# Kernel tuning notes

Hardware: AMD Instinct MI355X
Metric: run time of the kernel (lower is better)

The kernel has to match this reference:

```python
import jax, jax.numpy as jnp
import numpy as np

D_MODEL = 512
N_HEADS = 8
B, S = 2, 2048


def setup_inputs() -> dict:
    key = jax.random.key(0)
    ks = jax.random.split(key, 7)
    scale = 1.0 / np.sqrt(D_MODEL)
    return {
        "q": jax.random.normal(ks[0], (B, S, D_MODEL), jnp.float32),
        "k": jax.random.normal(ks[1], (B, S, D_MODEL), jnp.float32),
        "v": jax.random.normal(ks[2], (B, S, D_MODEL), jnp.float32),
        "Wq_w": jax.random.normal(ks[3], (D_MODEL, D_MODEL), jnp.float32) * scale,
        "Wq_b": jnp.zeros((D_MODEL,), jnp.float32),
        "Wc_w": jax.random.normal(ks[4], (D_MODEL, D_MODEL), jnp.float32) * scale,
        "Wc_b": jnp.zeros((D_MODEL,), jnp.float32),
    }


def _split(x, n_heads):
    b, s, d = x.shape
    return x.reshape(b, s, n_heads, d // n_heads).transpose(0, 2, 1, 3)  # [b,h,s,dh]


def reference(q, k, v, Wq_w, Wq_b, Wc_w, Wc_b):
    # NOTE: original code (faithfully) projects q, k, v all with W_q.
    qp = q @ Wq_w.T + Wq_b
    kp = k @ Wq_w.T + Wq_b
    vp = v @ Wq_w.T + Wq_b
    qh = _split(qp, N_HEADS)  # [b,h,s,dh]
    kh = _split(kp, N_HEADS)
    vh = _split(vp, N_HEADS)
    d_tensor = qh.shape[-1]
    scores = jnp.einsum("bhqd,bhkd->bhqk", qh, kh) / jnp.sqrt(jnp.float32(d_tensor))
    att = jax.nn.softmax(scores, axis=-1)
    out = jnp.einsum("bhqk,bhkd->bhqd", att, vh)
    b, h, s, dh = out.shape
    out = out.transpose(0, 2, 1, 3).reshape(b, s, h * dh)
    return out @ Wc_w.T + Wc_b
```

## Files before the change

kernel.cpp:

```cpp
#include <hip/hip_runtime.h>
#include <hip/hip_bf16.h>
#include <stdint.h>


typedef __bf16 bf16;
typedef __bf16 bvec8 __attribute__((ext_vector_type(8)));
typedef __bf16 bvec4 __attribute__((ext_vector_type(4)));
typedef float  fvec4 __attribute__((ext_vector_type(4)));
typedef float  fvec16 __attribute__((ext_vector_type(16)));
typedef int    ivec4 __attribute__((ext_vector_type(4)));

#define MFMA16(a, b, c) __builtin_amdgcn_mfma_f32_16x16x32_bf16(a, b, c, 0, 0, 0)
#define MFMA32(a, b, c) __builtin_amdgcn_mfma_f32_32x32x16_bf16(a, b, c, 0, 0, 0)

__device__ __forceinline__ void async16(const void* g, void* l) {
  __builtin_amdgcn_global_load_lds(
      (__attribute__((address_space(1))) void*)(g),
      (__attribute__((address_space(3))) void*)(l), 16, 0, 0);
}

__global__ void cvt_all(const float* __restrict__ q, const float* __restrict__ k,
                        const float* __restrict__ v, const float* __restrict__ Wq,
                        const float* __restrict__ Wc, bf16* __restrict__ qkvb,
                        bf16* __restrict__ Wq16, bf16* __restrict__ Wc16) {
  const int t = blockIdx.x * 256 + threadIdx.x;
  const float* src;
  bf16* dst;
  size_t i;
  if (t < 786432) {
    const int which = t >> 18;
    i = (size_t)(t & 262143);
    src = (which == 0) ? q : (which == 1) ? k : v;
    dst = qkvb + ((size_t)which << 21);
  } else if (t < 819200) {
    src = Wq; dst = Wq16; i = (size_t)(t - 786432);
  } else {
    src = Wc; dst = Wc16; i = (size_t)(t - 819200);
  }
  fvec4 a = *(const fvec4*)(src + i * 8);
  fvec4 b = *(const fvec4*)(src + i * 8 + 4);
  bvec8 o;
#pragma unroll
  for (int j = 0; j < 4; ++j) { o[j] = (bf16)a[j]; o[j + 4] = (bf16)b[j]; }
  *(bvec8*)(dst + i * 8) = o;
}

__launch_bounds__(256, 3)
__global__ void proj_gemm(const bf16* __restrict__ X, const bf16* __restrict__ W,
                          const float* __restrict__ bias, bf16* __restrict__ Y,
                          bf16* __restrict__ Yt) {
  __shared__ __attribute__((aligned(16))) char As[2][64 * 128];
  __shared__ __attribute__((aligned(16))) char Bs[2][128 * 128];

  const int tid = threadIdx.x;
  const int w = tid >> 6, l = tid & 63;
  const int wr = w >> 1, wc = w & 1;
  const int l15 = l & 15, lg = l >> 4;
  const int bm0 = blockIdx.x * 64;
  const int bn0 = blockIdx.y * 128;

  fvec4 acc[2][4] = {};

  auto stageA = [&](int buf, int k0) {
#pragma unroll
    for (int j = 0; j < 2; ++j) {
      int c = j * 256 + tid;
      int row = c >> 3, g = (c & 7) ^ (row & 7);
      async16(X + (size_t)(bm0 + row) * 512 + k0 + g * 8, &As[buf][c * 16]);
    }
  };
  auto stageB = [&](int buf, int k0) {
#pragma unroll
    for (int j = 0; j < 4; ++j) {
      int c = j * 256 + tid;
      int row = c >> 3, g = (c & 7) ^ (row & 7);
      async16(W + (size_t)(bn0 + row) * 512 + k0 + g * 8, &Bs[buf][c * 16]);
    }
  };

  stageA(0, 0);
  stageB(0, 0);
  __syncthreads();

  for (int t = 0; t < 8; ++t) {
    const int buf = t & 1;
    if (t < 7) { stageA(buf ^ 1, (t + 1) * 64); stageB(buf ^ 1, (t + 1) * 64); }
#pragma unroll
    for (int kk = 0; kk < 2; ++kk) {
      bvec8 af[2], bfr[4];
      const int g = kk * 4 + lg;
#pragma unroll
      for (int m = 0; m < 2; ++m) {
        int r = wr * 32 + m * 16 + l15;
        af[m] = *(const bvec8*)&As[buf][r * 128 + ((g ^ (r & 7)) << 4)];
      }
#pragma unroll
      for (int n = 0; n < 4; ++n) {
        int r = wc * 64 + n * 16 + l15;
        bfr[n] = *(const bvec8*)&Bs[buf][r * 128 + ((g ^ (r & 7)) << 4)];
      }
#pragma unroll
      for (int m = 0; m < 2; ++m)
#pragma unroll
        for (int n = 0; n < 4; ++n) acc[m][n] = MFMA16(af[m], bfr[n], acc[m][n]);
    }
    __syncthreads();
  }

  const bool trans = (bm0 >= 8192);
#pragma unroll
  for (int n = 0; n < 4; ++n) {
    const int col = bn0 + wc * 64 + n * 16 + l15;
    const float bv = bias[col];
#pragma unroll
    for (int m = 0; m < 2; ++m) {
      const int row0 = bm0 + wr * 32 + m * 16 + lg * 4;
      if (!trans) {
#pragma unroll
        for (int r = 0; r < 4; ++r)
          Y[(size_t)(row0 + r) * 512 + col] = (bf16)(acc[m][n][r] + bv);
      } else {
        const int m0 = row0 - 8192;
        const int b = m0 >> 11, s = m0 & 2047;
        bvec4 v4;
#pragma unroll
        for (int r = 0; r < 4; ++r) v4[r] = (bf16)(acc[m][n][r] + bv);
        *(bvec4*)&Yt[(size_t)(b * 512 + col) * 2048 + s] = v4;
      }
    }
  }
}

__launch_bounds__(256, 4)
__global__ void attn_kernel(const bf16* __restrict__ qp, const bf16* __restrict__ kp,
                            const bf16* __restrict__ vt, bf16* __restrict__ po01,
                            bf16* __restrict__ po23, float* __restrict__ pl) {
  __shared__ __attribute__((aligned(16))) char Ks[2][64 * 128];
  __shared__ __attribute__((aligned(16))) char Vs[2][64 * 128];

  const int tid = threadIdx.x;
  const int w = tid >> 6, l = tid & 63;
  const int l31 = l & 31, hi = l >> 5;

  const int lin = blockIdx.x;
  const int work = (lin & 7) * 128 + (lin >> 3);
  const int qb = work & 15, bh = (work >> 4) & 15, half = work >> 8;
  const int b = bh >> 3, h = bh & 7;
  const int kvbase = half * 512;
  const int qw0 = qb * 128 + w * 32;

  const bf16* kbase = kp + (size_t)(b * 2048) * 512 + h * 64;
  const bf16* vbase = vt + (size_t)(b * 512 + h * 64) * 2048;

  bvec8 qf[4];
  {
    const bf16* qrow = qp + (size_t)(b * 2048 + qw0 + l31) * 512 + h * 64 + hi * 8;
#pragma unroll
    for (int ks = 0; ks < 4; ++ks) qf[ks] = *(const bvec8*)(qrow + ks * 16);
  }

  auto stageK = [&](int buf, int kv0) {
#pragma unroll
    for (int j = 0; j < 2; ++j) {
      int c = j * 256 + tid;
      int row = c >> 3, g = (c & 7) ^ (row & 7);
      async16(kbase + (size_t)(kv0 + row) * 512 + g * 8, &Ks[buf][c * 16]);
    }
  };
  auto stageV = [&](int buf, int kv0) {
#pragma unroll
    for (int j = 0; j < 2; ++j) {
      int c = j * 256 + tid;
      int row = c >> 3, g = (c & 7) ^ (row & 7);
      async16(vbase + (size_t)row * 2048 + kv0 + g * 8, &Vs[buf][c * 16]);
    }
  };

  fvec16 oacc[2] = {};
  float l_run = 0.f;

  stageK(0, kvbase);
  stageV(0, kvbase);
  __syncthreads();

  const float SC = 0.125f * 1.44269504089f;

  for (int t = 0; t < 8; ++t) {
    const int buf = t & 1;
    if (t < 7) {
      stageK(buf ^ 1, kvbase + (t + 1) * 64);
      stageV(buf ^ 1, kvbase + (t + 1) * 64);
    }

    fvec16 sac[2] = {};
    __builtin_amdgcn_s_setprio(1);
#pragma unroll
    for (int ks = 0; ks < 4; ++ks) {
      const int chunk = ks * 2 + hi;
#pragma unroll
      for (int kvb = 0; kvb < 2; ++kvb) {
        const int r = kvb * 32 + l31;
        bvec8 kf = *(const bvec8*)&Ks[buf][r * 128 + ((chunk ^ (r & 7)) << 4)];
        sac[kvb] = MFMA32(kf, qf[ks], sac[kvb]);
      }
    }
    __builtin_amdgcn_s_setprio(0);

    ivec4 pw[4];
    float psum = 0.f;
#pragma unroll
    for (int f = 0; f < 2; ++f) {
      float p[16];
#pragma unroll
      for (int r2 = 0; r2 < 16; ++r2) {
        p[r2] = exp2f(sac[f][r2] * SC);
        psum += p[r2];
      }
      int wv[4][2];
#pragma unroll
      for (int m = 0; m < 4; ++m)
#pragma unroll
        for (int i = 0; i < 2; ++i)
          asm("v_cvt_pk_bf16_f32 %0, %1, %2"
              : "=v"(wv[m][i]) : "v"(p[4 * m + 2 * i]), "v"(p[4 * m + 2 * i + 1]));
#pragma unroll
      for (int i = 0; i < 2; ++i) {
        int a0 = wv[0][i], c0 = wv[1][i];
        asm volatile("v_permlane32_swap_b32 %0, %1" : "+v"(a0), "+v"(c0));
        pw[2 * f][i] = a0; pw[2 * f][2 + i] = c0;
        int a1 = wv[2][i], c1 = wv[3][i];
        asm volatile("v_permlane32_swap_b32 %0, %1" : "+v"(a1), "+v"(c1));
        pw[2 * f + 1][i] = a1; pw[2 * f + 1][2 + i] = c1;
      }
    }
    l_run += psum;

    __builtin_amdgcn_s_setprio(1);
#pragma unroll
    for (int ks = 0; ks < 4; ++ks) {
      const bvec8 pb = __builtin_bit_cast(bvec8, pw[ks]);
      const int chunk = ks * 2 + hi;
#pragma unroll
      for (int dhb = 0; dhb < 2; ++dhb) {
        const int r = dhb * 32 + l31;
        bvec8 vf = *(const bvec8*)&Vs[buf][r * 128 + ((chunk ^ (r & 7)) << 4)];
        oacc[dhb] = MFMA32(pb, vf, oacc[dhb]);
      }
    }
    __builtin_amdgcn_s_setprio(0);
    __syncthreads();
  }

  bf16* pob = ((half < 2) ? po01 : po23) + (size_t)(half & 1) * 2097152;
#pragma unroll
  for (int dhb = 0; dhb < 2; ++dhb)
#pragma unroll
    for (int r2 = 0; r2 < 16; ++r2) {
      const int q = qw0 + (r2 & 3) + 8 * (r2 >> 2) + 4 * hi;
      pob[(size_t)(b * 2048 + q) * 512 + h * 64 + dhb * 32 + l31] =
          (bf16)oacc[dhb][r2];
    }
  l_run += __shfl_xor(l_run, 32);
  if (hi == 0)
    pl[half * 32768 + (b * 2048 + qw0 + l31) * 8 + h] = l_run;
}

__launch_bounds__(256, 3)
__global__ void out_gemm(const bf16* __restrict__ po01, const bf16* __restrict__ po23,
                         const float* __restrict__ pl, const bf16* __restrict__ W,
                         const float* __restrict__ bias, float* __restrict__ Y) {
  __shared__ __attribute__((aligned(16))) char As[2][64 * 128];
  __shared__ __attribute__((aligned(16))) char Bs[2][128 * 128];

  const int tid = threadIdx.x;
  const int w = tid >> 6, l = tid & 63;
  const int wr = w >> 1, wc = w & 1;
  const int l15 = l & 15, lg = l >> 4;
  const int bm0 = blockIdx.x * 64;
  const int bn0 = blockIdx.y * 128;

  fvec4 acc[2][4] = {};

  bvec8 rp[2][4];
  fvec4 rl[2];

  auto loadA = [&](int k0) {
#pragma unroll
    for (int j = 0; j < 2; ++j) {
      int c = j * 256 + tid;
      int row = c >> 3, g = (c & 7) ^ (row & 7);
      const size_t off = (size_t)(bm0 + row) * 512 + k0 + g * 8;
      rp[j][0] = *(const bvec8*)(po01 + off);
      rp[j][1] = *(const bvec8*)(po01 + 2097152 + off);
      rp[j][2] = *(const bvec8*)(po23 + off);
      rp[j][3] = *(const bvec8*)(po23 + 2097152 + off);
      const int ridx = (bm0 + row) * 8 + ((k0 + g * 8) >> 6);
      rl[j] = fvec4{pl[ridx], pl[32768 + ridx], pl[65536 + ridx], pl[98304 + ridx]};
    }
  };
  auto writeA = [&](int buf) {
#pragma unroll
    for (int j = 0; j < 2; ++j) {
      int c = j * 256 + tid;
      const float inv = 1.0f / (rl[j][0] + rl[j][1] + rl[j][2] + rl[j][3]);
      bvec8 o;
#pragma unroll
      for (int e = 0; e < 8; ++e)
        o[e] = (bf16)((((float)rp[j][0][e] + (float)rp[j][1][e]) +
                       ((float)rp[j][2][e] + (float)rp[j][3][e])) * inv);
      *(bvec8*)&As[buf][c * 16] = o;
    }
  };
  auto stageB = [&](int buf, int k0) {
#pragma unroll
    for (int j = 0; j < 4; ++j) {
      int c = j * 256 + tid;
      int row = c >> 3, g = (c & 7) ^ (row & 7);
      async16(W + (size_t)(bn0 + row) * 512 + k0 + g * 8, &Bs[buf][c * 16]);
    }
  };

  loadA(0);
  stageB(0, 0);
  writeA(0);
  __syncthreads();

  for (int t = 0; t < 8; ++t) {
    const int buf = t & 1;
    if (t < 7) {
      loadA((t + 1) * 64);
      stageB(buf ^ 1, (t + 1) * 64);
    }
#pragma unroll
    for (int kk = 0; kk < 2; ++kk) {
      bvec8 af[2], bfr[4];
      const int g = kk * 4 + lg;
#pragma unroll
      for (int m = 0; m < 2; ++m) {
        int r = wr * 32 + m * 16 + l15;
        af[m] = *(const bvec8*)&As[buf][r * 128 + ((g ^ (r & 7)) << 4)];
      }
#pragma unroll
      for (int n = 0; n < 4; ++n) {
        int r = wc * 64 + n * 16 + l15;
        bfr[n] = *(const bvec8*)&Bs[buf][r * 128 + ((g ^ (r & 7)) << 4)];
      }
#pragma unroll
      for (int m = 0; m < 2; ++m)
#pragma unroll
        for (int n = 0; n < 4; ++n) acc[m][n] = MFMA16(af[m], bfr[n], acc[m][n]);
    }
    if (t < 7) writeA(buf ^ 1);
    __syncthreads();
  }

#pragma unroll
  for (int n = 0; n < 4; ++n) {
    const int col = bn0 + wc * 64 + n * 16 + l15;
    const float bv = bias[col];
#pragma unroll
    for (int m = 0; m < 2; ++m) {
      const int row0 = bm0 + wr * 32 + m * 16 + lg * 4;
#pragma unroll
      for (int r = 0; r < 4; ++r)
        Y[(size_t)(row0 + r) * 512 + col] = acc[m][n][r] + bv;
    }
  }
}

extern "C" void kernel_launch(void* const* d_in, const int* in_sizes, int n_in,
                              void* d_out, int out_size, void* d_ws, size_t ws_size,
                              hipStream_t stream) {
  const float* q   = (const float*)d_in[0];
  const float* k   = (const float*)d_in[1];
  const float* v   = (const float*)d_in[2];
  const float* Wq  = (const float*)d_in[3];
  const float* Wqb = (const float*)d_in[4];
  const float* Wc  = (const float*)d_in[5];
  const float* Wcb = (const float*)d_in[6];
  float* out = (float*)d_out;

  char* ws = (char*)d_ws;
  const size_t MB = 1u << 20;
  bf16* qkvb = (bf16*)(ws);
  bf16* po01 = (bf16*)(ws);
  bf16* Wq16 = (bf16*)(ws + 12 * MB);
  bf16* Wc16 = (bf16*)(ws + 12 * MB + 512 * 1024);
  bf16* qkp  = (bf16*)(ws + 13 * MB);
  bf16* vt   = (bf16*)(ws + 21 * MB);
  bf16* po23 = (bf16*)(ws + 25 * MB);
  float* pl  = (float*)(ws + 33 * MB);

  dim3 bb(256);
  hipLaunchKernelGGL(cvt_all, dim3(3328), bb, 0, stream, q, k, v, Wq, Wc,
                     qkvb, Wq16, Wc16);
  hipLaunchKernelGGL(proj_gemm, dim3(192, 4), bb, 0, stream,
                     qkvb, Wq16, Wqb, qkp, vt);
  hipLaunchKernelGGL(attn_kernel, dim3(1024), bb, 0, stream,
                     qkp, qkp + 2097152, vt, po01, po23, pl);
  hipLaunchKernelGGL(out_gemm, dim3(64, 4), bb, 0, stream,
                     po01, po23, pl, Wc16, Wcb, out);
}
```

Measured before the change: 72.36 us.

## Fold softmax scale into Q projection, MFMA row sums, separate combine kernel

Folds the softmax scale and log2e factor into the Q projection epilogue so the attention loop no longer multiplies scores. Row sums of the probabilities are now computed with an extra MFMA against a ones vector instead of scalar adds. The split-KV combine moves from the out_gemm A-load path into a standalone combine kernel, so out_gemm can load A asynchronously. The attention grid also changes from a swizzled 1D launch to a plain 3D launch. In exchange there is an extra kernel launch and an extra round trip of the combined activation through memory, and the swizzled block order is lost.

```diff
diff --git a/kernel.cpp b/kernel.cpp
--- a/kernel.cpp
+++ b/kernel.cpp
@@ -108,6 +108,7 @@
   }
 
   const bool trans = (bm0 >= 8192);
+  const float scl = (bm0 < 4096) ? 0.18033688011112042f : 1.0f;
 #pragma unroll
   for (int n = 0; n < 4; ++n) {
     const int col = bn0 + wc * 64 + n * 16 + l15;
@@ -118,7 +119,7 @@
       if (!trans) {
 #pragma unroll
         for (int r = 0; r < 4; ++r)
-          Y[(size_t)(row0 + r) * 512 + col] = (bf16)(acc[m][n][r] + bv);
+          Y[(size_t)(row0 + r) * 512 + col] = (bf16)((acc[m][n][r] + bv) * scl);
       } else {
         const int m0 = row0 - 8192;
         const int b = m0 >> 11, s = m0 & 2047;
@@ -141,13 +142,10 @@
   const int tid = threadIdx.x;
   const int w = tid >> 6, l = tid & 63;
   const int l31 = l & 31, hi = l >> 5;
-
-  const int lin = blockIdx.x;
-  const int work = (lin & 7) * 128 + (lin >> 3);
-  const int qb = work & 15, bh = (work >> 4) & 15, half = work >> 8;
-  const int b = bh >> 3, h = bh & 7;
+  const int bh = blockIdx.y, b = bh >> 3, h = bh & 7;
+  const int half = blockIdx.z;
   const int kvbase = half * 512;
-  const int qw0 = qb * 128 + w * 32;
+  const int qw0 = blockIdx.x * 128 + w * 32;
 
   const bf16* kbase = kp + (size_t)(b * 2048) * 512 + h * 64;
   const bf16* vbase = vt + (size_t)(b * 512 + h * 64) * 2048;
@@ -158,6 +156,9 @@
 #pragma unroll
     for (int ks = 0; ks < 4; ++ks) qf[ks] = *(const bvec8*)(qrow + ks * 16);
   }
+  bvec8 ones;
+#pragma unroll
+  for (int e = 0; e < 8; ++e) ones[e] = (bf16)1.0f;
 
   auto stageK = [&](int buf, int kv0) {
 #pragma unroll
@@ -177,13 +178,11 @@
   };
 
   fvec16 oacc[2] = {};
-  float l_run = 0.f;
+  fvec16 lacc = {};
 
   stageK(0, kvbase);
   stageV(0, kvbase);
   __syncthreads();
-
-  const float SC = 0.125f * 1.44269504089f;
 
   for (int t = 0; t < 8; ++t) {
     const int buf = t & 1;
@@ -207,15 +206,11 @@
     __builtin_amdgcn_s_setprio(0);
 
     ivec4 pw[4];
-    float psum = 0.f;
 #pragma unroll
     for (int f = 0; f < 2; ++f) {
       float p[16];
 #pragma unroll
-      for (int r2 = 0; r2 < 16; ++r2) {
-        p[r2] = exp2f(sac[f][r2] * SC);
-        psum += p[r2];
-      }
+      for (int r2 = 0; r2 < 16; ++r2) p[r2] = exp2f(sac[f][r2]);
       int wv[4][2];
 #pragma unroll
       for (int m = 0; m < 4; ++m)
@@ -233,7 +228,6 @@
         pw[2 * f + 1][i] = a1; pw[2 * f + 1][2 + i] = c1;
       }
     }
-    l_run += psum;
 
     __builtin_amdgcn_s_setprio(1);
 #pragma unroll
@@ -246,6 +240,7 @@
         bvec8 vf = *(const bvec8*)&Vs[buf][r * 128 + ((chunk ^ (r & 7)) << 4)];
         oacc[dhb] = MFMA32(pb, vf, oacc[dhb]);
       }
+      lacc = MFMA32(pb, ones, lacc);
     }
     __builtin_amdgcn_s_setprio(0);
     __syncthreads();
@@ -260,14 +255,36 @@
       pob[(size_t)(b * 2048 + q) * 512 + h * 64 + dhb * 32 + l31] =
           (bf16)oacc[dhb][r2];
     }
-  l_run += __shfl_xor(l_run, 32);
-  if (hi == 0)
-    pl[half * 32768 + (b * 2048 + qw0 + l31) * 8 + h] = l_run;
+  if (l31 == 0) {
+#pragma unroll
+    for (int r2 = 0; r2 < 16; ++r2) {
+      const int q = qw0 + (r2 & 3) + 8 * (r2 >> 2) + 4 * hi;
+      pl[half * 32768 + (b * 2048 + q) * 8 + h] = lacc[r2];
+    }
+  }
+}
+
+__global__ void combine_kernel(const bf16* __restrict__ po01, const bf16* __restrict__ po23,
+                               const float* __restrict__ pl, bf16* __restrict__ att) {
+  const int t = blockIdx.x * 256 + threadIdx.x;
+  const int row = t >> 6;
+  const int c8 = (t & 63) << 3;
+  const int h = c8 >> 6;
+  const float inv = 1.0f / (pl[row * 8 + h] + pl[32768 + row * 8 + h] +
+                            pl[65536 + row * 8 + h] + pl[98304 + row * 8 + h]);
+  bvec8 a0 = *(const bvec8*)(po01 + (size_t)row * 512 + c8);
+  bvec8 a1 = *(const bvec8*)(po01 + 2097152 + (size_t)row * 512 + c8);
+  bvec8 a2 = *(const bvec8*)(po23 + (size_t)row * 512 + c8);
+  bvec8 a3 = *(const bvec8*)(po23 + 2097152 + (size_t)row * 512 + c8);
+  bvec8 o;
+#pragma unroll
+  for (int j = 0; j < 8; ++j)
+    o[j] = (bf16)((((float)a0[j] + (float)a1[j]) + ((float)a2[j] + (float)a3[j])) * inv);
+  *(bvec8*)(att + (size_t)row * 512 + c8) = o;
 }
 
 __launch_bounds__(256, 3)
-__global__ void out_gemm(const bf16* __restrict__ po01, const bf16* __restrict__ po23,
-                         const float* __restrict__ pl, const bf16* __restrict__ W,
+__global__ void out_gemm(const bf16* __restrict__ X, const bf16* __restrict__ W,
                          const float* __restrict__ bias, float* __restrict__ Y) {
   __shared__ __attribute__((aligned(16))) char As[2][64 * 128];
   __shared__ __attribute__((aligned(16))) char Bs[2][128 * 128];
@@ -281,34 +298,12 @@
 
   fvec4 acc[2][4] = {};
 
-  bvec8 rp[2][4];
-  fvec4 rl[2];
-
-  auto loadA = [&](int k0) {
+  auto stageA = [&](int buf, int k0) {
 #pragma unroll
     for (int j = 0; j < 2; ++j) {
       int c = j * 256 + tid;
       int row = c >> 3, g = (c & 7) ^ (row & 7);
-      const size_t off = (size_t)(bm0 + row) * 512 + k0 + g * 8;
-      rp[j][0] = *(const bvec8*)(po01 + off);
-      rp[j][1] = *(const bvec8*)(po01 + 2097152 + off);
-      rp[j][2] = *(const bvec8*)(po23 + off);
-      rp[j][3] = *(const bvec8*)(po23 + 2097152 + off);
-      const int ridx = (bm0 + row) * 8 + ((k0 + g * 8) >> 6);
-      rl[j] = fvec4{pl[ridx], pl[32768 + ridx], pl[65536 + ridx], pl[98304 + ridx]};
-    }
-  };
-  auto writeA = [&](int buf) {
-#pragma unroll
-    for (int j = 0; j < 2; ++j) {
-      int c = j * 256 + tid;
-      const float inv = 1.0f / (rl[j][0] + rl[j][1] + rl[j][2] + rl[j][3]);
-      bvec8 o;
-#pragma unroll
-      for (int e = 0; e < 8; ++e)
-        o[e] = (bf16)((((float)rp[j][0][e] + (float)rp[j][1][e]) +
-                       ((float)rp[j][2][e] + (float)rp[j][3][e])) * inv);
-      *(bvec8*)&As[buf][c * 16] = o;
+      async16(X + (size_t)(bm0 + row) * 512 + k0 + g * 8, &As[buf][c * 16]);
     }
   };
   auto stageB = [&](int buf, int k0) {
@@ -320,17 +315,13 @@
     }
   };
 
-  loadA(0);
+  stageA(0, 0);
   stageB(0, 0);
-  writeA(0);
   __syncthreads();
 
   for (int t = 0; t < 8; ++t) {
     const int buf = t & 1;
-    if (t < 7) {
-      loadA((t + 1) * 64);
-      stageB(buf ^ 1, (t + 1) * 64);
-    }
+    if (t < 7) { stageA(buf ^ 1, (t + 1) * 64); stageB(buf ^ 1, (t + 1) * 64); }
 #pragma unroll
     for (int kk = 0; kk < 2; ++kk) {
       bvec8 af[2], bfr[4];
@@ -350,7 +341,6 @@
 #pragma unroll
         for (int n = 0; n < 4; ++n) acc[m][n] = MFMA16(af[m], bfr[n], acc[m][n]);
     }
-    if (t < 7) writeA(buf ^ 1);
     __syncthreads();
   }
 
@@ -384,6 +374,7 @@
   const size_t MB = 1u << 20;
   bf16* qkvb = (bf16*)(ws);
   bf16* po01 = (bf16*)(ws);
+  bf16* att  = (bf16*)(ws + 8 * MB);
   bf16* Wq16 = (bf16*)(ws + 12 * MB);
   bf16* Wc16 = (bf16*)(ws + 12 * MB + 512 * 1024);
   bf16* qkp  = (bf16*)(ws + 13 * MB);
@@ -396,8 +387,10 @@
                      qkvb, Wq16, Wc16);
   hipLaunchKernelGGL(proj_gemm, dim3(192, 4), bb, 0, stream,
                      qkvb, Wq16, Wqb, qkp, vt);
-  hipLaunchKernelGGL(attn_kernel, dim3(1024), bb, 0, stream,
+  hipLaunchKernelGGL(attn_kernel, dim3(16, 16, 4), bb, 0, stream,
                      qkp, qkp + 2097152, vt, po01, po23, pl);
+  hipLaunchKernelGGL(combine_kernel, dim3(1024), bb, 0, stream,
+                     po01, po23, pl, att);
   hipLaunchKernelGGL(out_gemm, dim3(64, 4), bb, 0, stream,
-                     po01, po23, pl, Wc16, Wcb, out);
-}
+                     att, Wc16, Wcb, out);
+}
```

New measurement: 71.31 us. About the same (-1.4%).
